# Kernel optimization log

Hardware: AMD Instinct MI355X
Metric: run time of the kernel (lower is better)

The kernel has to match this reference:

```python
import math
import jax, jax.numpy as jnp
import numpy as np

BATCH = 65536
SIZE = 1024


def _even_odd_mult(p, x):
    """(1-p)*x + p*[evens..., odds...] for x of shape (B, n)."""
    B, n = x.shape
    sep = x.reshape(B, n // 2, 2).transpose(0, 2, 1).reshape(B, n)
    return (1 - p) * x + p * sep


def _reverse_mult(p1, p2, x):
    """Probabilistically reverse first half (p1) and second half (p2)."""
    B, n = x.shape
    h = n // 2
    first = x[:, :h]
    second = x[:, h:]
    first = (1 - p1) * first + p1 * first[:, ::-1]
    second = (1 - p2) * second + p2 * second[:, ::-1]
    return jnp.concatenate([first, second], axis=-1)


def setup_inputs() -> dict:
    key = jax.random.key(0)
    k1, k2 = jax.random.split(key)
    x = jax.random.normal(k1, (BATCH, SIZE), dtype=jnp.float32)
    m = int(math.log2(SIZE))
    logits = jax.random.normal(k2, (m - 1, 3), dtype=jnp.float32)
    return {"x": x, "logits": logits}


def reference(x, logits):
    size = x.shape[-1]
    m = int(math.log2(size))
    # factor i has size sizes[i]; increasing_size=True -> [4, 8, ..., size]
    sizes = [size >> i for i in range(m - 1)][::-1]
    out = x
    # forward iterates factors[::-1]: largest block size first
    for i in range(m - 2, -1, -1):
        n = sizes[i]
        prob = jax.nn.sigmoid(logits[i])
        y = out.reshape(-1, n)
        y = _even_odd_mult(prob[0], y)
        y = _reverse_mult(prob[1], prob[2], y)
        out = y.reshape(out.shape)
    return out
```

## Files before the change

### kernel.cpp

```cpp
#include <hip/hip_runtime.h>
#include <math.h>

#define TPB 256

__device__ __forceinline__ unsigned swz(unsigned A) {
    return A ^ ((((A >> 8) ^ (A >> 11)) & 7u) << 4);
}

__device__ __forceinline__ float4 ldsrd(const char* ldsb, unsigned A) {
    return *(const float4*)(ldsb + A);
}

template<int N>
__device__ __forceinline__ void lds_stage(char* ldsb, unsigned rb, unsigned tt,
                                          float p, float p1, float p2) {
    constexpr unsigned H = N / 2;
    constexpr int L2 = (N == 512) ? 4 : (N == 256) ? 3 : 2;
    const unsigned b  = tt >> L2;
    const unsigned s  = tt & ((N / 32) - 1);
    const unsigned u0 = s * 8u;
    const unsigned bc = b * (unsigned)N;

    const unsigned Aj0  = swz(rb + 4u * (bc + u0));
    const unsigned Aj1  = swz(rb + 4u * (bc + H + u0));
    const unsigned Ajm0 = swz(rb + 4u * (bc + H - 8 - u0));
    const unsigned Ajm1 = swz(rb + 4u * (bc + N - 8 - u0));
    const unsigned Ae   = swz(rb + 4u * (bc + 2 * u0));
    const unsigned Aem  = swz(rb + 4u * (bc + 2 * H - 16 - 2 * u0));

    float j0[8], j1[8], jm0[8], jm1[8], e[16], em[16];
    *(float4*)&j0[0]  = ldsrd(ldsb, Aj0);        *(float4*)&j0[4]  = ldsrd(ldsb, Aj0 ^ 16u);
    *(float4*)&j1[0]  = ldsrd(ldsb, Aj1);        *(float4*)&j1[4]  = ldsrd(ldsb, Aj1 ^ 16u);
    *(float4*)&jm0[0] = ldsrd(ldsb, Ajm0);       *(float4*)&jm0[4] = ldsrd(ldsb, Ajm0 ^ 16u);
    *(float4*)&jm1[0] = ldsrd(ldsb, Ajm1);       *(float4*)&jm1[4] = ldsrd(ldsb, Ajm1 ^ 16u);
    *(float4*)&e[0]   = ldsrd(ldsb, Ae);         *(float4*)&e[4]   = ldsrd(ldsb, Ae ^ 16u);
    *(float4*)&e[8]   = ldsrd(ldsb, Ae ^ 32u);   *(float4*)&e[12]  = ldsrd(ldsb, Ae ^ 48u);
    *(float4*)&em[0]  = ldsrd(ldsb, Aem);        *(float4*)&em[4]  = ldsrd(ldsb, Aem ^ 16u);
    *(float4*)&em[8]  = ldsrd(ldsb, Aem ^ 32u);  *(float4*)&em[12] = ldsrd(ldsb, Aem ^ 48u);

    #pragma unroll
    for (int du = 0; du < 8; ++du) {
        {
            float yj = j0[du], yjm = jm0[7 - du];
            float yej = e[2 * du], yejm = em[14 - 2 * du];
            float a0 = fmaf(p, yej - yj, yj);
            float a1 = fmaf(p, yejm - yjm, yjm);
            float d  = a1 - a0;
            j0[du]      = fmaf(p1, d, a0);
            jm0[7 - du] = fmaf(p1, -d, a1);
        }
        {
            float zj = j1[du], zjm = jm1[7 - du];
            float zej = e[2 * du + 1], zejm = em[15 - 2 * du];
            float a0 = fmaf(p, zej - zj, zj);
            float a1 = fmaf(p, zejm - zjm, zjm);
            float d  = a1 - a0;
            j1[du]      = fmaf(p2, d, a0);
            jm1[7 - du] = fmaf(p2, -d, a1);
        }
    }
    __syncthreads();
    *(float4*)(ldsb + Aj0)          = *(const float4*)&j0[0];
    *(float4*)(ldsb + (Aj0 ^ 16u))  = *(const float4*)&j0[4];
    *(float4*)(ldsb + Aj1)          = *(const float4*)&j1[0];
    *(float4*)(ldsb + (Aj1 ^ 16u))  = *(const float4*)&j1[4];
    *(float4*)(ldsb + Ajm0)         = *(const float4*)&jm0[0];
    *(float4*)(ldsb + (Ajm0 ^ 16u)) = *(const float4*)&jm0[4];
    *(float4*)(ldsb + Ajm1)         = *(const float4*)&jm1[0];
    *(float4*)(ldsb + (Ajm1 ^ 16u)) = *(const float4*)&jm1[4];
    __syncthreads();
}

template<int N>
__device__ __forceinline__ void reg_stage(float* arr, float p, float p1, float p2) {
    constexpr int H = N / 2;
    float tmp[32];
    #pragma unroll
    for (int bb = 0; bb < 32; bb += N) {
        #pragma unroll
        for (int u = 0; u < N / 4; ++u) {
            {
                int j = bb + u, jm = bb + H - 1 - u;
                int ej = bb + 2 * u, ejm = bb + 2 * H - 2 - 2 * u;
                float a0 = fmaf(p, arr[ej]  - arr[j],  arr[j]);
                float a1 = fmaf(p, arr[ejm] - arr[jm], arr[jm]);
                tmp[j]  = fmaf(p1, a1 - a0, a0);
                tmp[jm] = fmaf(p1, a0 - a1, a1);
            }
            {
                int j = bb + H + u, jm = bb + 2 * H - 1 - u;
                int ej = bb + 2 * u + 1, ejm = bb + 2 * H - 1 - 2 * u;
                float a0 = fmaf(p, arr[ej]  - arr[j],  arr[j]);
                float a1 = fmaf(p, arr[ejm] - arr[jm], arr[jm]);
                tmp[j]  = fmaf(p2, a1 - a0, a0);
                tmp[jm] = fmaf(p2, a0 - a1, a1);
            }
        }
    }
    #pragma unroll
    for (int v = 0; v < 32; ++v) arr[v] = tmp[v];
}

__global__ void bpp_prep(const float* __restrict__ logits, float* __restrict__ sp) {
    int i = threadIdx.x;
    if (i < 27) sp[i] = 1.0f / (1.0f + expf(-logits[i]));
}

template<bool USE_WS>
__global__ __launch_bounds__(TPB) void bpp_main(const float* __restrict__ x,
                                                float* __restrict__ out,
                                                const float* __restrict__ spws,
                                                const float* __restrict__ logits) {
    __shared__ float lds[8 * 1024];
    char* ldsb = (char*)lds;
    const unsigned t = threadIdx.x;
    const size_t gbase = (size_t)blockIdx.x * (8 * 1024);

    float prl[27];
    if constexpr (!USE_WS) {
        #pragma unroll
        for (int i = 0; i < 27; ++i) prl[i] = 1.0f / (1.0f + expf(-logits[i]));
    }
    #define PV(i) (USE_WS ? spws[(i)] : prl[(i)])

    {
        const unsigned row = t >> 5, tt = t & 31u;
        const unsigned rb = row * 4096u;
        const float* __restrict__ gr = x + gbase + row * 1024u;
        const float p = PV(24), p1 = PV(25), p2 = PV(26);

        float j0[8], j1[8], jm0[8], jm1[8], e[16], em[16];
        #define LD4(dst, off) *(float4*)&(dst) = *(const float4*)(gr + (off))
        LD4(j0[0],  8u * tt);            LD4(j0[4],  8u * tt + 4u);
        LD4(j1[0],  512u + 8u * tt);     LD4(j1[4],  516u + 8u * tt);
        LD4(jm0[0], 504u - 8u * tt);     LD4(jm0[4], 508u - 8u * tt);
        LD4(jm1[0], 1016u - 8u * tt);    LD4(jm1[4], 1020u - 8u * tt);
        LD4(e[0],   16u * tt);           LD4(e[4],   16u * tt + 4u);
        LD4(e[8],   16u * tt + 8u);      LD4(e[12],  16u * tt + 12u);
        LD4(em[0],  1008u - 16u * tt);   LD4(em[4],  1012u - 16u * tt);
        LD4(em[8],  1016u - 16u * tt);   LD4(em[12], 1020u - 16u * tt);
        #undef LD4

        #pragma unroll
        for (int du = 0; du < 8; ++du) {
            {
                float yj = j0[du], yjm = jm0[7 - du];
                float yej = e[2 * du], yejm = em[14 - 2 * du];
                float a0 = fmaf(p, yej - yj, yj);
                float a1 = fmaf(p, yejm - yjm, yjm);
                float d  = a1 - a0;
                j0[du]      = fmaf(p1, d, a0);
                jm0[7 - du] = fmaf(p1, -d, a1);
            }
            {
                float zj = j1[du], zjm = jm1[7 - du];
                float zej = e[2 * du + 1], zejm = em[15 - 2 * du];
                float a0 = fmaf(p, zej - zj, zj);
                float a1 = fmaf(p, zejm - zjm, zjm);
                float d  = a1 - a0;
                j1[du]      = fmaf(p2, d, a0);
                jm1[7 - du] = fmaf(p2, -d, a1);
            }
        }
        const unsigned Aj0  = swz(rb + 32u * tt);
        const unsigned Aj1  = swz(rb + 2048u + 32u * tt);
        const unsigned Ajm0 = swz(rb + 2016u - 32u * tt);
        const unsigned Ajm1 = swz(rb + 4064u - 32u * tt);
        *(float4*)(ldsb + Aj0)          = *(const float4*)&j0[0];
        *(float4*)(ldsb + (Aj0 ^ 16u))  = *(const float4*)&j0[4];
        *(float4*)(ldsb + Aj1)          = *(const float4*)&j1[0];
        *(float4*)(ldsb + (Aj1 ^ 16u))  = *(const float4*)&j1[4];
        *(float4*)(ldsb + Ajm0)         = *(const float4*)&jm0[0];
        *(float4*)(ldsb + (Ajm0 ^ 16u)) = *(const float4*)&jm0[4];
        *(float4*)(ldsb + Ajm1)         = *(const float4*)&jm1[0];
        *(float4*)(ldsb + (Ajm1 ^ 16u)) = *(const float4*)&jm1[4];
    }
    __syncthreads();

    {
        const unsigned row = t >> 5, tt = t & 31u;
        const unsigned rb = row * 4096u;
        lds_stage<512>(ldsb, rb, tt, PV(21), PV(22), PV(23));
        lds_stage<256>(ldsb, rb, tt, PV(18), PV(19), PV(20));
        lds_stage<128>(ldsb, rb, tt, PV(15), PV(16), PV(17));
    }

    {
        const unsigned r5 = t & 7u, b5 = (t >> 3) & 15u, h5 = t >> 7;
        const unsigned base = r5 * 4096u + b5 * 256u + h5 * 128u;
        const unsigned So = swz(base);
        const unsigned St = So ^ 128u;
        float own[32], oth[32];
        #pragma unroll
        for (int k = 0; k < 8; ++k) {
            *(float4*)&own[4 * k] = ldsrd(ldsb, So ^ (16u * k));
            *(float4*)&oth[4 * k] = ldsrd(ldsb, St ^ (16u * k));
        }
        const float p = PV(12), p1 = PV(13), p2 = PV(14);
        float o[32];
        if (h5 == 0) {
            #pragma unroll
            for (int u = 0; u < 16; ++u) {
                float yj = own[u], yjm = own[31 - u];
                float a0 = fmaf(p, own[2 * u] - yj, yj);
                float a1 = fmaf(p, oth[30 - 2 * u] - yjm, yjm);
                float d  = a1 - a0;
                o[u]      = fmaf(p1, d, a0);
                o[31 - u] = fmaf(p1, -d, a1);
            }
        } else {
            #pragma unroll
            for (int u = 0; u < 16; ++u) {
                float yj = own[u], yjm = own[31 - u];
                float a0 = fmaf(p, oth[2 * u + 1] - yj, yj);
                float a1 = fmaf(p, own[31 - 2 * u] - yjm, yjm);
                float d  = a1 - a0;
                o[u]      = fmaf(p2, d, a0);
                o[31 - u] = fmaf(p2, -d, a1);
            }
        }
        reg_stage<32>(o, PV(9), PV(10), PV(11));
        reg_stage<16>(o, PV(6), PV(7),  PV(8));
        reg_stage< 8>(o, PV(3), PV(4),  PV(5));
        reg_stage< 4>(o, PV(0), PV(1),  PV(2));

        float* __restrict__ go = out + gbase + r5 * 1024u + b5 * 64u + h5 * 32u;
        #pragma unroll
        for (int k = 0; k < 8; ++k)
            *(float4*)(go + 4 * k) = *(const float4*)&o[4 * k];
    }
    #undef PV
}

extern "C" void kernel_launch(void* const* d_in, const int* in_sizes, int n_in,
                              void* d_out, int out_size, void* d_ws, size_t ws_size,
                              hipStream_t stream) {
    const float* x      = (const float*)d_in[0];
    const float* logits = (const float*)d_in[1];
    float* out = (float*)d_out;
    int rows = in_sizes[0] / 1024;
    int grid = rows / 8;
    if (ws_size >= 27 * sizeof(float)) {
        float* sp = (float*)d_ws;
        bpp_prep<<<dim3(1), dim3(32), 0, stream>>>(logits, sp);
        bpp_main<true><<<dim3(grid), dim3(TPB), 0, stream>>>(x, out, sp, logits);
    } else {
        bpp_main<false><<<dim3(grid), dim3(TPB), 0, stream>>>(x, out, nullptr, logits);
    }
}
```

Measured before the change: 154.1 us.

## Drop block barriers by keeping each LDS row inside one wavefront

```diff
diff --git a/kernel.cpp b/kernel.cpp
--- a/kernel.cpp
+++ b/kernel.cpp
@@ -59,7 +59,6 @@
             jm1[7 - du] = fmaf(p2, -d, a1);
         }
     }
-    __syncthreads();
     *(float4*)(ldsb + Aj0)          = *(const float4*)&j0[0];
     *(float4*)(ldsb + (Aj0 ^ 16u))  = *(const float4*)&j0[4];
     *(float4*)(ldsb + Aj1)          = *(const float4*)&j1[0];
@@ -68,7 +67,6 @@
     *(float4*)(ldsb + (Ajm0 ^ 16u)) = *(const float4*)&jm0[4];
     *(float4*)(ldsb + Ajm1)         = *(const float4*)&jm1[0];
     *(float4*)(ldsb + (Ajm1 ^ 16u)) = *(const float4*)&jm1[4];
-    __syncthreads();
 }
 
 template<int N>
@@ -123,9 +121,11 @@
     }
     #define PV(i) (USE_WS ? spws[(i)] : prl[(i)])
 
+    const unsigned w = t >> 6, l = t & 63u;
+    const unsigned row = t >> 5, tt = t & 31u;
+    const unsigned rb = row * 4096u;
+
     {
-        const unsigned row = t >> 5, tt = t & 31u;
-        const unsigned rb = row * 4096u;
         const float* __restrict__ gr = x + gbase + row * 1024u;
         const float p = PV(24), p1 = PV(25), p2 = PV(26);
 
@@ -175,18 +175,16 @@
         *(float4*)(ldsb + Ajm1)         = *(const float4*)&jm1[0];
         *(float4*)(ldsb + (Ajm1 ^ 16u)) = *(const float4*)&jm1[4];
     }
-    __syncthreads();
+
+    lds_stage<512>(ldsb, rb, tt, PV(21), PV(22), PV(23));
+    lds_stage<256>(ldsb, rb, tt, PV(18), PV(19), PV(20));
+    lds_stage<128>(ldsb, rb, tt, PV(15), PV(16), PV(17));
 
     {
-        const unsigned row = t >> 5, tt = t & 31u;
-        const unsigned rb = row * 4096u;
-        lds_stage<512>(ldsb, rb, tt, PV(21), PV(22), PV(23));
-        lds_stage<256>(ldsb, rb, tt, PV(18), PV(19), PV(20));
-        lds_stage<128>(ldsb, rb, tt, PV(15), PV(16), PV(17));
-    }
-
-    {
-        const unsigned r5 = t & 7u, b5 = (t >> 3) & 15u, h5 = t >> 7;
+        const unsigned m5 = l & 31u;
+        const unsigned r5 = 2u * w + (m5 & 1u);
+        const unsigned b5 = m5 >> 1;
+        const unsigned h5 = l >> 5;
         const unsigned base = r5 * 4096u + b5 * 256u + h5 * 128u;
         const unsigned So = swz(base);
         const unsigned St = So ^ 128u;
@@ -196,28 +194,19 @@
             *(float4*)&own[4 * k] = ldsrd(ldsb, So ^ (16u * k));
             *(float4*)&oth[4 * k] = ldsrd(ldsb, St ^ (16u * k));
         }
-        const float p = PV(12), p1 = PV(13), p2 = PV(14);
+        const float p = PV(12);
+        const float q64 = h5 ? PV(14) : PV(13);
         float o[32];
-        if (h5 == 0) {
-            #pragma unroll
-            for (int u = 0; u < 16; ++u) {
-                float yj = own[u], yjm = own[31 - u];
-                float a0 = fmaf(p, own[2 * u] - yj, yj);
-                float a1 = fmaf(p, oth[30 - 2 * u] - yjm, yjm);
-                float d  = a1 - a0;
-                o[u]      = fmaf(p1, d, a0);
-                o[31 - u] = fmaf(p1, -d, a1);
-            }
-        } else {
-            #pragma unroll
-            for (int u = 0; u < 16; ++u) {
-                float yj = own[u], yjm = own[31 - u];
-                float a0 = fmaf(p, oth[2 * u + 1] - yj, yj);
-                float a1 = fmaf(p, own[31 - 2 * u] - yjm, yjm);
-                float d  = a1 - a0;
-                o[u]      = fmaf(p2, d, a0);
-                o[31 - u] = fmaf(p2, -d, a1);
-            }
+        #pragma unroll
+        for (int u = 0; u < 16; ++u) {
+            float eja = h5 ? oth[2 * u + 1]  : own[2 * u];
+            float ejb = h5 ? own[31 - 2 * u] : oth[30 - 2 * u];
+            float yj = own[u], yjm = own[31 - u];
+            float a0 = fmaf(p, eja - yj, yj);
+            float a1 = fmaf(p, ejb - yjm, yjm);
+            float d  = a1 - a0;
+            o[u]      = fmaf(q64, d, a0);
+            o[31 - u] = fmaf(q64, -d, a1);
         }
         reg_stage<32>(o, PV(9), PV(10), PV(11));
         reg_stage<16>(o, PV(6), PV(7),  PV(8));
```

New measurement: 158.3 us. +2.7%, slower.
